# Performance work log

Hardware: AMD Instinct MI355X
Metric: run time of the kernel (lower is better)

The kernel has to match this reference:

```python
import jax, jax.numpy as jnp
import numpy as np

L, B, T = 512, 1024, 48

def setup_inputs() -> dict:
    key = jax.random.key(0)
    k0, k1, k2, k3, k4 = jax.random.split(key, 5)
    emissions = jax.random.normal(k0, (L, B, T), dtype=jnp.float32)
    tags = jax.random.randint(k1, (L, B), 0, T)
    mask = jnp.ones((L, B), dtype=jnp.int32)
    start_transitions = 0.1 * jax.random.normal(k2, (T,), dtype=jnp.float32)
    end_transitions = 0.1 * jax.random.normal(k3, (T,), dtype=jnp.float32)
    transitions = 0.1 * jax.random.normal(k4, (T, T), dtype=jnp.float32)
    return {"emissions": emissions, "tags": tags, "mask": mask,
            "start_transitions": start_transitions,
            "end_transitions": end_transitions,
            "transitions": transitions}


def _crf_llh(emissions, tags, mask, start_transitions, end_transitions, transitions):
    seq_len, batch, num_tags = emissions.shape
    maskf = mask.astype(emissions.dtype)

    # ---- numerator: joint log-likelihood of the gold tag path ----
    # emission score of the gold tag at each position: (L, B)
    emis_at_tags = jnp.take_along_axis(emissions, tags[:, :, None], axis=2)[:, :, 0]
    llh = start_transitions[tags[0]]                                  # (B,)
    llh = llh + jnp.sum(emis_at_tags[:-1] * maskf[:-1], axis=0)       # emissions for t=0..L-2
    trans_scores = transitions[tags[:-1], tags[1:]]                   # (L-1, B)
    llh = llh + jnp.sum(trans_scores * maskf[1:], axis=0)
    last_idx = jnp.sum(mask, axis=0).astype(jnp.int32) - 1            # (B,)
    last_tags = tags[last_idx, jnp.arange(batch)]                     # (B,)
    llh = llh + end_transitions[last_tags]
    llh = llh + emissions[-1][jnp.arange(batch), last_tags] * maskf[-1]

    # ---- denominator: log partition function via log-sum-exp scan ----
    def step(log_prob, x):
        e_t, m_t = x  # (B, T), (B,)
        # score[b, j] = logsumexp_i( log_prob[b, i] + trans[i, j] ) + e_t[b, j]
        score = jax.nn.logsumexp(log_prob[:, :, None] + transitions[None, :, :], axis=1) + e_t
        log_prob = jnp.where(m_t[:, None] > 0, score, log_prob)
        return log_prob, None

    init = start_transitions[None, :] + emissions[0]                  # (B, T)
    log_prob, _ = jax.lax.scan(step, init, (emissions[1:], maskf[1:]))
    log_z = jax.nn.logsumexp(log_prob + end_transitions[None, :], axis=1)  # (B,)

    return jnp.sum(llh - log_z)  # summed=True


def reference(emissions, tags, mask, start_transitions, end_transitions, transitions):
    return _crf_llh(emissions, tags, mask, start_transitions, end_transitions, transitions)
```

## Files before the change

kernel.cpp:

```cpp
#include <hip/hip_runtime.h>

#define Lq 512
#define Bn 1024
#define Tq 48

typedef float f32x4 __attribute__((ext_vector_type(4)));
typedef short s16x8 __attribute__((ext_vector_type(8)));

#define MFMA(a, b, c) __builtin_amdgcn_mfma_f32_16x16x32_bf16((a), (b), (c), 0, 0, 0)

__device__ __forceinline__ unsigned cvtpk(float lo, float hi) {
    unsigned r;
    asm("v_cvt_pk_bf16_f32 %0, %1, %2" : "=v"(r) : "v"(lo), "v"(hi));
    return r;
}
__device__ __forceinline__ short f2b(float x) {
    unsigned u = __float_as_uint(x);
    return (short)((u + 0x7fffu + ((u >> 16) & 1u)) >> 16);
}

#define STEP(EA, EB, EC, MV, RS) do {                                         \
    f32x4 C0_ = MFMA(aw00, Bk0, Zf); C0_ = MFMA(aw01, Bk1, C0_);              \
    f32x4 C1_ = MFMA(aw10, Bk0, Zf); C1_ = MFMA(aw11, Bk1, C1_);              \
    f32x4 C2_ = MFMA(aw20, Bk0, Zf); C2_ = MFMA(aw21, Bk1, C2_);              \
    if ((MV) != 0) {                                                          \
        pn0[0]=C0_[0]*__expf((EA)[0]); pn0[1]=C0_[1]*__expf((EA)[1]);         \
        pn0[2]=C0_[2]*__expf((EA)[2]); pn0[3]=C0_[3]*__expf((EA)[3]);         \
        pn1[0]=C1_[0]*__expf((EB)[0]); pn1[1]=C1_[1]*__expf((EB)[1]);         \
        pn1[2]=C1_[2]*__expf((EB)[2]); pn1[3]=C1_[3]*__expf((EB)[3]);         \
        pn2[0]=C2_[0]*__expf((EC)[0]); pn2[1]=C2_[1]*__expf((EC)[1]);         \
        pn2[2]=C2_[2]*__expf((EC)[2]); pn2[3]=C2_[3]*__expf((EC)[3]);         \
    }                                                                         \
    if (RS) {                                                                 \
        float rep_ = __shfl(pn0[0], cidx, 64);         \
        int k_ = ((__float_as_int(rep_) >> 23) & 0xff) - 126;                 \
        float scl_ = __int_as_float((127 - k_) << 23);                        \
        pn0[0]*=scl_; pn0[1]*=scl_; pn0[2]*=scl_; pn0[3]*=scl_;               \
        pn1[0]*=scl_; pn1[1]*=scl_; pn1[2]*=scl_; pn1[3]*=scl_;               \
        pn2[0]*=scl_; pn2[1]*=scl_; pn2[2]*=scl_; pn2[3]*=scl_;               \
        c2 += k_;                                                             \
    }                                                                         \
    *(uint2*)(ldsc + wr0) = make_uint2(cvtpk(pn0[0],pn0[1]), cvtpk(pn0[2],pn0[3])); \
    *(uint2*)(ldsc + wr1) = make_uint2(cvtpk(pn1[0],pn1[1]), cvtpk(pn1[2],pn1[3])); \
    *(uint2*)(ldsc + wr2) = make_uint2(cvtpk(pn2[0],pn2[1]), cvtpk(pn2[2],pn2[3])); \
    Bk0 = *(const s16x8*)(ldsc + rd0);                                        \
    Bk1 = *(const s16x8*)(ldsc + rd1);                                        \
} while (0)

#define LOAD_SLOT(D, T) do {                                                  \
    int t_ = (T); int v_ = (t_ < Lq); int tc_ = v_ ? t_ : (Lq - 1);           \
    const float* ep_ = em + ((size_t)tc_ * Bn + bidx) * Tq;                   \
    ea_##D = *(const f32x4*)(ep_ + 4 * qidx);                                 \
    eb_##D = *(const f32x4*)(ep_ + 16 + 4 * qidx);                            \
    ec_##D = *(const f32x4*)(ep_ + 32 + 4 * qidx);                            \
    m_##D  = v_ ? mask[tc_ * Bn + bidx] : 0;                                  \
} while (0)

__global__ __launch_bounds__(64) void crf_forward(
    const float* __restrict__ em, const int* __restrict__ mask,
    const float* __restrict__ startT, const float* __restrict__ endT,
    const float* __restrict__ trans, float* __restrict__ out)
{
    const int j = threadIdx.x;
    const int cidx = j & 15;
    const int qidx = j >> 4;
    const int b0 = blockIdx.x * 16;
    const int bidx = b0 + cidx;

    __shared__ float shf[2304];
    char* ldsc = (char*)shf;

    for (int i = j; i < Tq * Tq; i += 64) shf[i] = trans[i];
    __syncthreads();
    s16x8 aw00, aw01, aw10, aw11, aw20, aw21;
#pragma unroll
    for (int i = 0; i < 8; ++i) {
        int so0 = qidx * 8 + i;
        int so1 = 32 + qidx * 8 + i;
        aw00[i] = f2b(__expf(shf[so0 * Tq + cidx]));
        aw10[i] = f2b(__expf(shf[so0 * Tq + 16 + cidx]));
        aw20[i] = f2b(__expf(shf[so0 * Tq + 32 + cidx]));
        float w01 = so1 < Tq ? __expf(shf[so1 * Tq + cidx]) : 0.f;
        float w11 = so1 < Tq ? __expf(shf[so1 * Tq + 16 + cidx]) : 0.f;
        float w21 = so1 < Tq ? __expf(shf[so1 * Tq + 32 + cidx]) : 0.f;
        aw01[i] = f2b(w01); aw11[i] = f2b(w11); aw21[i] = f2b(w21);
    }
    __syncthreads();

    if (j < 16) *(uint4*)(ldsc + j * 112 + 96) = make_uint4(0, 0, 0, 0);
    if (j == 16) *(uint4*)(ldsc + 1792) = make_uint4(0, 0, 0, 0);

    f32x4 pn0, pn1, pn2;
    {
        const float* e0p = em + (size_t)bidx * Tq;
        f32x4 ea = *(const f32x4*)(e0p + 4 * qidx);
        f32x4 eb = *(const f32x4*)(e0p + 16 + 4 * qidx);
        f32x4 ec = *(const f32x4*)(e0p + 32 + 4 * qidx);
#pragma unroll
        for (int i = 0; i < 4; ++i) {
            pn0[i] = __expf(startT[ 0 + 4 * qidx + i] + ea[i]);
            pn1[i] = __expf(startT[16 + 4 * qidx + i] + eb[i]);
            pn2[i] = __expf(startT[32 + 4 * qidx + i] + ec[i]);
        }
    }

    const int wr0 = cidx * 112 + qidx * 8;
    const int wr1 = cidx * 112 + 32 + qidx * 8;
    const int wr2 = cidx * 112 + 64 + qidx * 8;
    const int rd0 = cidx * 112 + 16 * qidx;
    const int rd1 = (qidx == 3) ? 1792 : (cidx * 112 + 64 + 16 * qidx);
    const f32x4 Zf = {0.f, 0.f, 0.f, 0.f};
    int c2 = 0;

    *(uint2*)(ldsc + wr0) = make_uint2(cvtpk(pn0[0], pn0[1]), cvtpk(pn0[2], pn0[3]));
    *(uint2*)(ldsc + wr1) = make_uint2(cvtpk(pn1[0], pn1[1]), cvtpk(pn1[2], pn1[3]));
    *(uint2*)(ldsc + wr2) = make_uint2(cvtpk(pn2[0], pn2[1]), cvtpk(pn2[2], pn2[3]));
    __syncthreads();
    s16x8 Bk0 = *(const s16x8*)(ldsc + rd0);
    s16x8 Bk1 = *(const s16x8*)(ldsc + rd1);

    f32x4 ea_0, eb_0, ec_0, ea_1, eb_1, ec_1;
    f32x4 ea_2, eb_2, ec_2, ea_3, eb_3, ec_3;
    int m_0, m_1, m_2, m_3;
    LOAD_SLOT(0, 1); LOAD_SLOT(1, 2); LOAD_SLOT(2, 3); LOAD_SLOT(3, 4);

    for (int ch = 0; ch < 128; ++ch) {
        const int tb = 1 + 4 * ch;
        STEP(ea_0, eb_0, ec_0, m_0, 0); LOAD_SLOT(0, tb + 4);
        STEP(ea_1, eb_1, ec_1, m_1, 0); LOAD_SLOT(1, tb + 5);
        STEP(ea_2, eb_2, ec_2, m_2, 0); LOAD_SLOT(2, tb + 6);
        STEP(ea_3, eb_3, ec_3, m_3, 1); LOAD_SLOT(3, tb + 7);
    }

    float zacc = 0.f;
#pragma unroll
    for (int i = 0; i < 4; ++i) {
        zacc += pn0[i] * __expf(endT[ 0 + 4 * qidx + i]);
        zacc += pn1[i] * __expf(endT[16 + 4 * qidx + i]);
        zacc += pn2[i] * __expf(endT[32 + 4 * qidx + i]);
    }
    zacc += __shfl_xor(zacc, 16, 64);
    zacc += __shfl_xor(zacc, 32, 64);
    float nl = -(__logf(zacc) + (float)c2 * 0.6931471805599453f);
    nl += __shfl_xor(nl, 1, 64);
    nl += __shfl_xor(nl, 2, 64);
    nl += __shfl_xor(nl, 4, 64);
    nl += __shfl_xor(nl, 8, 64);
    if (j == 0) atomicAdd(out, nl);
}

__global__ __launch_bounds__(256) void crf_llh(
    const float* __restrict__ em, const int* __restrict__ tags,
    const int* __restrict__ mask, const float* __restrict__ startT,
    const float* __restrict__ endT, const float* __restrict__ trans,
    float* __restrict__ out)
{
    float c = 0.0f;
    for (int id = blockIdx.x * blockDim.x + threadIdx.x; id < Lq * Bn;
         id += gridDim.x * blockDim.x) {
        int t  = id >> 10;
        int bb = id & (Bn - 1);
        int tag = tags[id];
        int m_t = mask[id];
        if (t == 0) c += startT[tag];
        bool is_last;
        if (t < Lq - 1) {
            if (m_t) c += em[(size_t)id * Tq + tag];
            int tag1 = tags[id + Bn];
            int m1   = mask[id + Bn];
            if (m1) c += trans[tag * Tq + tag1];
            is_last = (m_t != 0) && (m1 == 0);
        } else {
            is_last = (m_t != 0);
        }
        if (is_last) {
            c += endT[tag];
            int mL = mask[(Lq - 1) * Bn + bb];
            if (mL) c += em[((size_t)(Lq - 1) * Bn + bb) * Tq + tag];
        }
    }
#pragma unroll
    for (int off = 32; off >= 1; off >>= 1)
        c += __shfl_xor(c, off, 64);
    __shared__ float red[4];
    if ((threadIdx.x & 63) == 0) red[threadIdx.x >> 6] = c;
    __syncthreads();
    if (threadIdx.x == 0)
        atomicAdd(out, red[0] + red[1] + red[2] + red[3]);
}

extern "C" void kernel_launch(void* const* d_in, const int* in_sizes, int n_in,
                              void* d_out, int out_size, void* d_ws, size_t ws_size,
                              hipStream_t stream) {
    const float* em     = (const float*)d_in[0];
    const int*   tags   = (const int*)d_in[1];
    const int*   mask   = (const int*)d_in[2];
    const float* startT = (const float*)d_in[3];
    const float* endT   = (const float*)d_in[4];
    const float* trans  = (const float*)d_in[5];
    float* out = (float*)d_out;

    hipMemsetAsync(out, 0, sizeof(float), stream);
    crf_llh<<<512, 256, 0, stream>>>(em, tags, mask, startT, endT, trans, out);
    crf_forward<<<64, 64, 0, stream>>>(em, mask, startT, endT, trans, out);
}
```

Baseline: 150.6 us.

## Keep CRF forward state in registers via MFMA layout and fuse both kernels

The forward recurrence no longer round-trips the probability vector through LDS each step. The transition weight fragments are reordered so that the MFMA accumulator layout maps directly onto the next step's B operand, which lets the packed bf16 values be fed straight back as registers. Masking becomes per-element selects instead of a branch. The numerator kernel is merged into the same launch as extra 64-thread blocks, which removes one kernel launch and lets the two parts overlap. The risk is that the register-layout reinterpretation must exactly match the MFMA lane mapping, and the numerator now runs as 512 single-wave blocks.

```diff
diff --git a/kernel.cpp b/kernel.cpp
--- a/kernel.cpp
+++ b/kernel.cpp
@@ -6,6 +6,7 @@
 
 typedef float f32x4 __attribute__((ext_vector_type(4)));
 typedef short s16x8 __attribute__((ext_vector_type(8)));
+typedef unsigned u32x4 __attribute__((ext_vector_type(4)));
 
 #define MFMA(a, b, c) __builtin_amdgcn_mfma_f32_16x16x32_bf16((a), (b), (c), 0, 0, 0)
 
@@ -19,32 +20,42 @@
     return (short)((u + 0x7fffu + ((u >> 16) & 1u)) >> 16);
 }
 
+#define PACKB do {                                                            \
+    unsigned d0_ = cvtpk(pn0[0], pn0[1]), d1_ = cvtpk(pn0[2], pn0[3]);        \
+    unsigned d2_ = cvtpk(pn1[0], pn1[1]), d3_ = cvtpk(pn1[2], pn1[3]);        \
+    unsigned d4_ = cvtpk(pn2[0], pn2[1]), d5_ = cvtpk(pn2[2], pn2[3]);        \
+    u32x4 b0_ = {d0_, d1_, d2_, d3_};                                         \
+    u32x4 b1_ = {d4_, d5_, 0u, 0u};                                           \
+    Bk0 = __builtin_bit_cast(s16x8, b0_);                                     \
+    Bk1 = __builtin_bit_cast(s16x8, b1_);                                     \
+} while (0)
+
 #define STEP(EA, EB, EC, MV, RS) do {                                         \
     f32x4 C0_ = MFMA(aw00, Bk0, Zf); C0_ = MFMA(aw01, Bk1, C0_);              \
     f32x4 C1_ = MFMA(aw10, Bk0, Zf); C1_ = MFMA(aw11, Bk1, C1_);              \
     f32x4 C2_ = MFMA(aw20, Bk0, Zf); C2_ = MFMA(aw21, Bk1, C2_);              \
-    if ((MV) != 0) {                                                          \
-        pn0[0]=C0_[0]*__expf((EA)[0]); pn0[1]=C0_[1]*__expf((EA)[1]);         \
-        pn0[2]=C0_[2]*__expf((EA)[2]); pn0[3]=C0_[3]*__expf((EA)[3]);         \
-        pn1[0]=C1_[0]*__expf((EB)[0]); pn1[1]=C1_[1]*__expf((EB)[1]);         \
-        pn1[2]=C1_[2]*__expf((EB)[2]); pn1[3]=C1_[3]*__expf((EB)[3]);         \
-        pn2[0]=C2_[0]*__expf((EC)[0]); pn2[1]=C2_[1]*__expf((EC)[1]);         \
-        pn2[2]=C2_[2]*__expf((EC)[2]); pn2[3]=C2_[3]*__expf((EC)[3]);         \
-    }                                                                         \
+    pn0[0] = (MV) ? C0_[0] * __expf((EA)[0]) : pn0[0];                        \
+    pn0[1] = (MV) ? C0_[1] * __expf((EA)[1]) : pn0[1];                        \
+    pn0[2] = (MV) ? C0_[2] * __expf((EA)[2]) : pn0[2];                        \
+    pn0[3] = (MV) ? C0_[3] * __expf((EA)[3]) : pn0[3];                        \
+    pn1[0] = (MV) ? C1_[0] * __expf((EB)[0]) : pn1[0];                        \
+    pn1[1] = (MV) ? C1_[1] * __expf((EB)[1]) : pn1[1];                        \
+    pn1[2] = (MV) ? C1_[2] * __expf((EB)[2]) : pn1[2];                        \
+    pn1[3] = (MV) ? C1_[3] * __expf((EB)[3]) : pn1[3];                        \
+    pn2[0] = (MV) ? C2_[0] * __expf((EC)[0]) : pn2[0];                        \
+    pn2[1] = (MV) ? C2_[1] * __expf((EC)[1]) : pn2[1];                        \
+    pn2[2] = (MV) ? C2_[2] * __expf((EC)[2]) : pn2[2];                        \
+    pn2[3] = (MV) ? C2_[3] * __expf((EC)[3]) : pn2[3];                        \
     if (RS) {                                                                 \
         float rep_ = __shfl(pn0[0], cidx, 64);         \
         int k_ = ((__float_as_int(rep_) >> 23) & 0xff) - 126;                 \
-        float scl_ = __int_as_float((127 - k_) << 23);                        \
+        float scl_ = __int_as_float((127 - k_) << 23);        \
         pn0[0]*=scl_; pn0[1]*=scl_; pn0[2]*=scl_; pn0[3]*=scl_;               \
         pn1[0]*=scl_; pn1[1]*=scl_; pn1[2]*=scl_; pn1[3]*=scl_;               \
         pn2[0]*=scl_; pn2[1]*=scl_; pn2[2]*=scl_; pn2[3]*=scl_;               \
         c2 += k_;                                                             \
     }                                                                         \
-    *(uint2*)(ldsc + wr0) = make_uint2(cvtpk(pn0[0],pn0[1]), cvtpk(pn0[2],pn0[3])); \
-    *(uint2*)(ldsc + wr1) = make_uint2(cvtpk(pn1[0],pn1[1]), cvtpk(pn1[2],pn1[3])); \
-    *(uint2*)(ldsc + wr2) = make_uint2(cvtpk(pn2[0],pn2[1]), cvtpk(pn2[2],pn2[3])); \
-    Bk0 = *(const s16x8*)(ldsc + rd0);                                        \
-    Bk1 = *(const s16x8*)(ldsc + rd1);                                        \
+    PACKB;                                                                    \
 } while (0)
 
 #define LOAD_SLOT(D, T) do {                                                  \
@@ -56,137 +67,116 @@
     m_##D  = v_ ? mask[tc_ * Bn + bidx] : 0;                                  \
 } while (0)
 
-__global__ __launch_bounds__(64) void crf_forward(
-    const float* __restrict__ em, const int* __restrict__ mask,
-    const float* __restrict__ startT, const float* __restrict__ endT,
-    const float* __restrict__ trans, float* __restrict__ out)
-{
-    const int j = threadIdx.x;
-    const int cidx = j & 15;
-    const int qidx = j >> 4;
-    const int b0 = blockIdx.x * 16;
-    const int bidx = b0 + cidx;
-
-    __shared__ float shf[2304];
-    char* ldsc = (char*)shf;
-
-    for (int i = j; i < Tq * Tq; i += 64) shf[i] = trans[i];
-    __syncthreads();
-    s16x8 aw00, aw01, aw10, aw11, aw20, aw21;
-#pragma unroll
-    for (int i = 0; i < 8; ++i) {
-        int so0 = qidx * 8 + i;
-        int so1 = 32 + qidx * 8 + i;
-        aw00[i] = f2b(__expf(shf[so0 * Tq + cidx]));
-        aw10[i] = f2b(__expf(shf[so0 * Tq + 16 + cidx]));
-        aw20[i] = f2b(__expf(shf[so0 * Tq + 32 + cidx]));
-        float w01 = so1 < Tq ? __expf(shf[so1 * Tq + cidx]) : 0.f;
-        float w11 = so1 < Tq ? __expf(shf[so1 * Tq + 16 + cidx]) : 0.f;
-        float w21 = so1 < Tq ? __expf(shf[so1 * Tq + 32 + cidx]) : 0.f;
-        aw01[i] = f2b(w01); aw11[i] = f2b(w11); aw21[i] = f2b(w21);
-    }
-    __syncthreads();
-
-    if (j < 16) *(uint4*)(ldsc + j * 112 + 96) = make_uint4(0, 0, 0, 0);
-    if (j == 16) *(uint4*)(ldsc + 1792) = make_uint4(0, 0, 0, 0);
-
-    f32x4 pn0, pn1, pn2;
-    {
-        const float* e0p = em + (size_t)bidx * Tq;
-        f32x4 ea = *(const f32x4*)(e0p + 4 * qidx);
-        f32x4 eb = *(const f32x4*)(e0p + 16 + 4 * qidx);
-        f32x4 ec = *(const f32x4*)(e0p + 32 + 4 * qidx);
-#pragma unroll
-        for (int i = 0; i < 4; ++i) {
-            pn0[i] = __expf(startT[ 0 + 4 * qidx + i] + ea[i]);
-            pn1[i] = __expf(startT[16 + 4 * qidx + i] + eb[i]);
-            pn2[i] = __expf(startT[32 + 4 * qidx + i] + ec[i]);
-        }
-    }
-
-    const int wr0 = cidx * 112 + qidx * 8;
-    const int wr1 = cidx * 112 + 32 + qidx * 8;
-    const int wr2 = cidx * 112 + 64 + qidx * 8;
-    const int rd0 = cidx * 112 + 16 * qidx;
-    const int rd1 = (qidx == 3) ? 1792 : (cidx * 112 + 64 + 16 * qidx);
-    const f32x4 Zf = {0.f, 0.f, 0.f, 0.f};
-    int c2 = 0;
-
-    *(uint2*)(ldsc + wr0) = make_uint2(cvtpk(pn0[0], pn0[1]), cvtpk(pn0[2], pn0[3]));
-    *(uint2*)(ldsc + wr1) = make_uint2(cvtpk(pn1[0], pn1[1]), cvtpk(pn1[2], pn1[3]));
-    *(uint2*)(ldsc + wr2) = make_uint2(cvtpk(pn2[0], pn2[1]), cvtpk(pn2[2], pn2[3]));
-    __syncthreads();
-    s16x8 Bk0 = *(const s16x8*)(ldsc + rd0);
-    s16x8 Bk1 = *(const s16x8*)(ldsc + rd1);
-
-    f32x4 ea_0, eb_0, ec_0, ea_1, eb_1, ec_1;
-    f32x4 ea_2, eb_2, ec_2, ea_3, eb_3, ec_3;
-    int m_0, m_1, m_2, m_3;
-    LOAD_SLOT(0, 1); LOAD_SLOT(1, 2); LOAD_SLOT(2, 3); LOAD_SLOT(3, 4);
-
-    for (int ch = 0; ch < 128; ++ch) {
-        const int tb = 1 + 4 * ch;
-        STEP(ea_0, eb_0, ec_0, m_0, 0); LOAD_SLOT(0, tb + 4);
-        STEP(ea_1, eb_1, ec_1, m_1, 0); LOAD_SLOT(1, tb + 5);
-        STEP(ea_2, eb_2, ec_2, m_2, 0); LOAD_SLOT(2, tb + 6);
-        STEP(ea_3, eb_3, ec_3, m_3, 1); LOAD_SLOT(3, tb + 7);
-    }
-
-    float zacc = 0.f;
-#pragma unroll
-    for (int i = 0; i < 4; ++i) {
-        zacc += pn0[i] * __expf(endT[ 0 + 4 * qidx + i]);
-        zacc += pn1[i] * __expf(endT[16 + 4 * qidx + i]);
-        zacc += pn2[i] * __expf(endT[32 + 4 * qidx + i]);
-    }
-    zacc += __shfl_xor(zacc, 16, 64);
-    zacc += __shfl_xor(zacc, 32, 64);
-    float nl = -(__logf(zacc) + (float)c2 * 0.6931471805599453f);
-    nl += __shfl_xor(nl, 1, 64);
-    nl += __shfl_xor(nl, 2, 64);
-    nl += __shfl_xor(nl, 4, 64);
-    nl += __shfl_xor(nl, 8, 64);
-    if (j == 0) atomicAdd(out, nl);
-}
-
-__global__ __launch_bounds__(256) void crf_llh(
+__global__ __launch_bounds__(64) void crf_fused(
     const float* __restrict__ em, const int* __restrict__ tags,
     const int* __restrict__ mask, const float* __restrict__ startT,
     const float* __restrict__ endT, const float* __restrict__ trans,
     float* __restrict__ out)
 {
-    float c = 0.0f;
-    for (int id = blockIdx.x * blockDim.x + threadIdx.x; id < Lq * Bn;
-         id += gridDim.x * blockDim.x) {
-        int t  = id >> 10;
-        int bb = id & (Bn - 1);
-        int tag = tags[id];
-        int m_t = mask[id];
-        if (t == 0) c += startT[tag];
-        bool is_last;
-        if (t < Lq - 1) {
-            if (m_t) c += em[(size_t)id * Tq + tag];
-            int tag1 = tags[id + Bn];
-            int m1   = mask[id + Bn];
-            if (m1) c += trans[tag * Tq + tag1];
-            is_last = (m_t != 0) && (m1 == 0);
-        } else {
-            is_last = (m_t != 0);
+    const int j = threadIdx.x;
+    __shared__ float shf[Tq * Tq];
+
+    if (blockIdx.x < 64) {
+        const int cidx = j & 15;
+        const int qidx = j >> 4;
+        const int bidx = blockIdx.x * 16 + cidx;
+
+        for (int i = j; i < Tq * Tq; i += 64) shf[i] = trans[i];
+        __syncthreads();
+        s16x8 aw00, aw01, aw10, aw11, aw20, aw21;
+#pragma unroll
+        for (int i = 0; i < 8; ++i) {
+            int l0 = (i < 4) ? (4 * qidx + i) : (12 + 4 * qidx + i);
+            aw00[i] = f2b(__expf(shf[l0 * Tq + cidx]));
+            aw10[i] = f2b(__expf(shf[l0 * Tq + 16 + cidx]));
+            aw20[i] = f2b(__expf(shf[l0 * Tq + 32 + cidx]));
+            if (i < 4) {
+                int l1 = 32 + 4 * qidx + i;
+                aw01[i] = f2b(__expf(shf[l1 * Tq + cidx]));
+                aw11[i] = f2b(__expf(shf[l1 * Tq + 16 + cidx]));
+                aw21[i] = f2b(__expf(shf[l1 * Tq + 32 + cidx]));
+            } else {
+                aw01[i] = 0; aw11[i] = 0; aw21[i] = 0;
+            }
         }
-        if (is_last) {
-            c += endT[tag];
-            int mL = mask[(Lq - 1) * Bn + bb];
-            if (mL) c += em[((size_t)(Lq - 1) * Bn + bb) * Tq + tag];
+
+        f32x4 pn0, pn1, pn2;
+        {
+            const float* e0p = em + (size_t)bidx * Tq;
+            f32x4 ea = *(const f32x4*)(e0p + 4 * qidx);
+            f32x4 eb = *(const f32x4*)(e0p + 16 + 4 * qidx);
+            f32x4 ec = *(const f32x4*)(e0p + 32 + 4 * qidx);
+#pragma unroll
+            for (int i = 0; i < 4; ++i) {
+                pn0[i] = __expf(startT[ 0 + 4 * qidx + i] + ea[i]);
+                pn1[i] = __expf(startT[16 + 4 * qidx + i] + eb[i]);
+                pn2[i] = __expf(startT[32 + 4 * qidx + i] + ec[i]);
+            }
         }
+
+        const f32x4 Zf = {0.f, 0.f, 0.f, 0.f};
+        s16x8 Bk0, Bk1;
+        int c2 = 0;
+        PACKB;
+
+        f32x4 ea_0, eb_0, ec_0, ea_1, eb_1, ec_1;
+        f32x4 ea_2, eb_2, ec_2, ea_3, eb_3, ec_3;
+        int m_0, m_1, m_2, m_3;
+        LOAD_SLOT(0, 1); LOAD_SLOT(1, 2); LOAD_SLOT(2, 3); LOAD_SLOT(3, 4);
+
+        for (int ch = 0; ch < 128; ++ch) {
+            const int tb = 1 + 4 * ch;
+            STEP(ea_0, eb_0, ec_0, m_0, 0); LOAD_SLOT(0, tb + 4);
+            STEP(ea_1, eb_1, ec_1, m_1, 0); LOAD_SLOT(1, tb + 5);
+            STEP(ea_2, eb_2, ec_2, m_2, 0); LOAD_SLOT(2, tb + 6);
+            STEP(ea_3, eb_3, ec_3, m_3, 1); LOAD_SLOT(3, tb + 7);
+        }
+
+        float zacc = 0.f;
+#pragma unroll
+        for (int i = 0; i < 4; ++i) {
+            zacc += pn0[i] * __expf(endT[ 0 + 4 * qidx + i]);
+            zacc += pn1[i] * __expf(endT[16 + 4 * qidx + i]);
+            zacc += pn2[i] * __expf(endT[32 + 4 * qidx + i]);
+        }
+        zacc += __shfl_xor(zacc, 16, 64);
+        zacc += __shfl_xor(zacc, 32, 64);
+        float nl = -(__logf(zacc) + (float)c2 * 0.6931471805599453f);
+        nl += __shfl_xor(nl, 1, 64);
+        nl += __shfl_xor(nl, 2, 64);
+        nl += __shfl_xor(nl, 4, 64);
+        nl += __shfl_xor(nl, 8, 64);
+        if (j == 0) atomicAdd(out, nl);
+    } else {
+        const int bid = blockIdx.x - 64;
+        float c = 0.0f;
+        for (int id = bid * 64 + j; id < Lq * Bn; id += 512 * 64) {
+            int t  = id >> 10;
+            int bb = id & (Bn - 1);
+            int tag = tags[id];
+            int m_t = mask[id];
+            if (t == 0) c += startT[tag];
+            bool is_last;
+            if (t < Lq - 1) {
+                if (m_t) c += em[(size_t)id * Tq + tag];
+                int tag1 = tags[id + Bn];
+                int m1   = mask[id + Bn];
+                if (m1) c += trans[tag * Tq + tag1];
+                is_last = (m_t != 0) && (m1 == 0);
+            } else {
+                is_last = (m_t != 0);
+            }
+            if (is_last) {
+                c += endT[tag];
+                int mL = mask[(Lq - 1) * Bn + bb];
+                if (mL) c += em[((size_t)(Lq - 1) * Bn + bb) * Tq + tag];
+            }
+        }
+#pragma unroll
+        for (int off = 32; off >= 1; off >>= 1)
+            c += __shfl_xor(c, off, 64);
+        if (j == 0) atomicAdd(out, c);
     }
-#pragma unroll
-    for (int off = 32; off >= 1; off >>= 1)
-        c += __shfl_xor(c, off, 64);
-    __shared__ float red[4];
-    if ((threadIdx.x & 63) == 0) red[threadIdx.x >> 6] = c;
-    __syncthreads();
-    if (threadIdx.x == 0)
-        atomicAdd(out, red[0] + red[1] + red[2] + red[3]);
 }
 
 extern "C" void kernel_launch(void* const* d_in, const int* in_sizes, int n_in,
@@ -201,6 +191,5 @@
     float* out = (float*)d_out;
 
     hipMemsetAsync(out, 0, sizeof(float), stream);
-    crf_llh<<<512, 256, 0, stream>>>(em, tags, mask, startT, endT, trans, out);
-    crf_forward<<<64, 64, 0, stream>>>(em, mask, startT, endT, trans, out);
+    crf_fused<<<576, 64, 0, stream>>>(em, tags, mask, startT, endT, trans, out);
 }
```

Result: faster. 137.9 us (-8.5%).
